# Kernel tuning notes

Hardware: AMD Instinct MI355X
Metric: run time of the kernel (lower is better)

## Reference

```python
import jax, jax.numpy as jnp
import numpy as np

VOXEL_SIZE = 0.4
GAMMA = 1.1  # VoxelPointsSampler.GAMMA
PC_MIN, PC_MAX = -75.2, 75.2


def setup_inputs() -> dict:
    key = jax.random.key(0)
    ks = jax.random.split(key, 6)
    N, M, C, S = 200000, 256, 5, 128
    xy = jax.random.uniform(ks[0], (N, 2), minval=PC_MIN, maxval=PC_MAX)
    z = jax.random.uniform(ks[1], (N, 1), minval=-2.0, maxval=4.0)
    feat = jax.random.normal(ks[2], (N, C - 3))
    points = jnp.concatenate([xy, z, feat], axis=1)  # [N, 5]
    ctr = jax.random.uniform(ks[3], (M, 2), minval=PC_MIN * 0.9, maxval=PC_MAX * 0.9)
    cz = jnp.zeros((M, 1), jnp.float32)
    dims = jax.random.uniform(ks[4], (M, 3), minval=1.0, maxval=5.0)
    yaw = jax.random.uniform(ks[5], (M, 1), minval=-3.14, maxval=3.14)
    boxes = jnp.concatenate([ctr, cz, dims, yaw], axis=1)  # [M, 7]
    pc_start = jnp.array([PC_MIN, PC_MIN], dtype=jnp.float32)
    return {"points": points, "boxes": boxes, "pc_start": pc_start, "num_sample": S}


def reference(points, boxes, pc_start, num_sample):
    N, C = points.shape
    M = boxes.shape[0]
    # --- voxel-level radius ball query (distances in voxel units) ---
    pcoords = (points[:, :2] - pc_start) / VOXEL_SIZE          # [N, 2]
    qcoords = (boxes[:, :2] - pc_start) / VOXEL_SIZE           # [M, 2]
    r_vox = jnp.linalg.norm(boxes[:, 3:5] * 0.5, axis=-1) * GAMMA / VOXEL_SIZE  # [M]
    dist = jnp.linalg.norm(qcoords[:, None, :] - pcoords[None, :, :], axis=-1)  # [M, N]
    vmask = (dist < r_vox[:, None]).any(axis=0)                # [N]
    # --- cylindrical pool (metric space); invalid points pushed out of every radius ---
    BIG = jnp.asarray(1e6, points.dtype)
    xy_m = jnp.where(vmask[:, None], points[:, :2], BIG)       # [N, 2]
    radii = jnp.linalg.norm(boxes[:, 3:5] * 0.5, axis=-1) * GAMMA  # [M]
    dis = jnp.linalg.norm(boxes[:, None, :2] - xy_m[None, :, :], axis=-1)  # [M, N]
    pmask = (dis <= radii[:, None]).astype(points.dtype)       # 0/1 [M, N]
    sm, sidx = jax.lax.top_k(pmask, num_sample)                # [M, S]
    smb = sm > 0.5                                             # bool [M, S]
    # unique indices across all sampled slots (fixed-size for jit)
    uniq, inv = jnp.unique(sidx.ravel(), return_inverse=True,
                           size=M * num_sample, fill_value=0)
    query_points = points[uniq]                                # [M*S, C] (padded)
    sampled_points = points[sidx] * smb[:, :, None]            # [M, S, C]
    idx = inv.reshape(M, num_sample).astype(jnp.int32) * smb   # [M, S]
    return sampled_points, idx, query_points
```

## Files before the change

kernel.cpp:

```cpp
#include <hip/hip_runtime.h>

typedef unsigned long long u64;
typedef unsigned short u16;
typedef unsigned char u8;

#define VOX 0.4f
#define GAM 1.1f
#define NCX 16
#define CELLW 32.0f
#define CAP 64

__device__ __forceinline__ float dist2d(float ax, float ay, float bx, float by) {
  float dx = __fsub_rn(ax, bx);
  float dy = __fsub_rn(ay, by);
  return __fsqrt_rn(__fadd_rn(__fmul_rn(dx, dx), __fmul_rn(dy, dy)));
}

__device__ __forceinline__ float box_radius(const float* __restrict__ boxes, int m) {
  float hx = __fmul_rn(boxes[m * 7 + 3], 0.5f);
  float hy = __fmul_rn(boxes[m * 7 + 4], 0.5f);
  float nr = __fsqrt_rn(__fadd_rn(__fmul_rn(hx, hx), __fmul_rn(hy, hy)));
  return __fmul_rn(nr, GAM);
}

__device__ __forceinline__ void box_voxel(const float* __restrict__ boxes, int m,
                                          float psx, float psy,
                                          float& qx, float& qy, float& r) {
  qx = __fdiv_rn(__fsub_rn(boxes[m * 7 + 0], psx), VOX);
  qy = __fdiv_rn(__fsub_rn(boxes[m * 7 + 1], psy), VOX);
  float hx = __fmul_rn(boxes[m * 7 + 3], 0.5f);
  float hy = __fmul_rn(boxes[m * 7 + 4], 0.5f);
  float nr = __fsqrt_rn(__fadd_rn(__fmul_rn(hx, hx), __fmul_rn(hy, hy)));
  r = __fdiv_rn(__fmul_rn(nr, GAM), VOX);
}

__global__ void k_prep(const float* __restrict__ boxes, const float* __restrict__ pc_start,
                       float* __restrict__ qxv, float* __restrict__ qyv, float* __restrict__ rv,
                       int* __restrict__ cellCnt, u16* __restrict__ cellList, int M) {
  const int tid = threadIdx.x;
  if (blockIdx.x == 0) {
    for (int m = tid; m < M; m += 256) {
      float qx, qy, r;
      box_voxel(boxes, m, pc_start[0], pc_start[1], qx, qy, r);
      qxv[m] = qx; qyv[m] = qy; rv[m] = r;
    }
    return;
  }
  const int cell = blockIdx.x - 1;
  const int cx = cell & (NCX - 1), cy = cell >> 4;
  const int wv = tid >> 6, lane = tid & 63;
  __shared__ int wcnt[4];
  const float x0 = (cx == 0) ? -3e38f : cx * CELLW;
  const float x1 = (cx == NCX - 1) ? 3e38f : (cx + 1) * CELLW;
  const float y0 = (cy == 0) ? -3e38f : cy * CELLW;
  const float y1 = (cy == NCX - 1) ? 3e38f : (cy + 1) * CELLW;
  bool hit = false;
  if (tid < M) {
    float qx, qy, r;
    box_voxel(boxes, tid, pc_start[0], pc_start[1], qx, qy, r);
    float ddx = fmaxf(0.0f, fmaxf(x0 - qx, qx - x1));
    float ddy = fmaxf(0.0f, fmaxf(y0 - qy, qy - y1));
    float rr = r + 0.01f;
    hit = (ddx * ddx + ddy * ddy <= rr * rr);
  }
  u64 b = __ballot(hit);
  if (lane == 0) wcnt[wv] = __popcll(b);
  __syncthreads();
  int base = 0;
  for (int w = 0; w < wv; ++w) base += wcnt[w];
  if (hit) {
    int slot = base + __popcll(b & ((1ULL << lane) - 1ULL));
    if (slot < CAP) cellList[cell * CAP + slot] = (u16)tid;
  }
  if (tid == 0) cellCnt[cell] = wcnt[0] + wcnt[1] + wcnt[2] + wcnt[3];
}

__global__ void k_vmask_count(const float* __restrict__ pts, const float* __restrict__ boxes,
                              const float* __restrict__ qxv, const float* __restrict__ qyv,
                              const float* __restrict__ rv,
                              const int* __restrict__ cellCnt, const u16* __restrict__ cellList,
                              u64* __restrict__ vbits, u8* __restrict__ present,
                              u64* __restrict__ bmG, int* __restrict__ cpng,
                              const float* __restrict__ pc_start,
                              int N, int M) {
  __shared__ float cpx[256], cpy[256];
  __shared__ int cpn[256];
  __shared__ float sbx[256], sby[256], sbr[256];
  __shared__ u64 bm[256][4];
  __shared__ int wcnt[4];
  const int tid = threadIdx.x;
  const int blk = blockIdx.x;
  const int n = blk * 256 + tid;
  const int wv = tid >> 6, lane = tid & 63;
  const float psx = pc_start[0], psy = pc_start[1];
  const bool valid = (n < N);

  bm[tid][0] = 0; bm[tid][1] = 0; bm[tid][2] = 0; bm[tid][3] = 0;
  if (tid < M) {
    sbx[tid] = boxes[tid * 7 + 0];
    sby[tid] = boxes[tid * 7 + 1];
    sbr[tid] = box_radius(boxes, tid);
  }

  float px = 1e6f, py = 1e6f, pvx = 0.f, pvy = 0.f;
  if (valid) {
    px = pts[n * 5 + 0];
    py = pts[n * 5 + 1];
    pvx = __fdiv_rn(__fsub_rn(px, psx), VOX);
    pvy = __fdiv_rn(__fsub_rn(py, psy), VOX);
    present[n] = 0;
  }

  bool flag = false;
  if (valid) {
    int cx = (int)floorf(pvx * (1.0f / CELLW));
    int cy = (int)floorf(pvy * (1.0f / CELLW));
    cx = cx < 0 ? 0 : (cx > NCX - 1 ? NCX - 1 : cx);
    cy = cy < 0 ? 0 : (cy > NCX - 1 ? NCX - 1 : cy);
    const int cell = cy * NCX + cx;
    const int k = cellCnt[cell];
    if (k <= CAP) {
      for (int j = 0; j < k; ++j) {
        const int m = cellList[cell * CAP + j];
        float d = dist2d(qxv[m], qyv[m], pvx, pvy);
        if (d < rv[m]) { flag = true; break; }
      }
    } else {
      for (int m = 0; m < M; ++m) {
        float d = dist2d(qxv[m], qyv[m], pvx, pvy);
        if (d < rv[m]) { flag = true; break; }
      }
    }
  }
  u64 b = __ballot(flag);
  if (lane == 0) {
    vbits[n >> 6] = b;
    wcnt[wv] = __popcll(b);
  }
  __syncthreads();

  int base = 0;
  for (int w = 0; w < wv; ++w) base += wcnt[w];
  if (flag) {
    int slot = base + __popcll(b & ((1ULL << lane) - 1ULL));
    cpx[slot] = px;
    cpy[slot] = py;
    cpn[slot] = n;
  }
  __syncthreads();
  const int nfl = wcnt[0] + wcnt[1] + wcnt[2] + wcnt[3];
  if (tid < nfl) cpng[blk * 256 + tid] = cpn[tid];

  if (tid < nfl) {
    const float mx = cpx[tid], my = cpy[tid];
    float vx = __fdiv_rn(__fsub_rn(mx, psx), VOX);
    float vy = __fdiv_rn(__fsub_rn(my, psy), VOX);
    int cx = (int)floorf(vx * (1.0f / CELLW));
    int cy = (int)floorf(vy * (1.0f / CELLW));
    cx = cx < 0 ? 0 : (cx > NCX - 1 ? NCX - 1 : cx);
    cy = cy < 0 ? 0 : (cy > NCX - 1 ? NCX - 1 : cy);
    const int cell = cy * NCX + cx;
    const int k = cellCnt[cell];
    const u64 bit = 1ULL << (tid & 63);
    const int word = tid >> 6;
    if (k <= CAP) {
      for (int j = 0; j < k; ++j) {
        const int m = cellList[cell * CAP + j];
        float d = dist2d(sbx[m], sby[m], mx, my);
        if (d <= sbr[m]) atomicOr(&bm[m][word], bit);
      }
    } else {
      for (int m = 0; m < M; ++m) {
        float d = dist2d(sbx[m], sby[m], mx, my);
        if (d <= sbr[m]) atomicOr(&bm[m][word], bit);
      }
    }
  }
  __syncthreads();

  if (tid < M) {
    u64* dst = bmG + ((size_t)blk * M + tid) * 4;
    dst[0] = bm[tid][0]; dst[1] = bm[tid][1];
    dst[2] = bm[tid][2]; dst[3] = bm[tid][3];
  }
}

__global__ void __launch_bounds__(1024) k_scanfill(
    const float* __restrict__ pts, const float* __restrict__ boxes,
    const u64* __restrict__ bmG, const int* __restrict__ cpng,
    const u64* __restrict__ vbits, int* __restrict__ kcount,
    int* __restrict__ sidx, u8* __restrict__ present,
    int N, int M, int S, int nchunk) {
  const int m = blockIdx.x;
  const int t = threadIdx.x;
  const int lane = t & 63, wv = t >> 6;
  __shared__ int wsum[16];
  __shared__ int zws[16];

  u64 w0 = 0, w1 = 0, w2 = 0, w3 = 0;
  int v = 0;
  if (t < nchunk) {
    const u64* bp = bmG + ((size_t)t * M + m) * 4;
    w0 = bp[0]; w1 = bp[1]; w2 = bp[2]; w3 = bp[3];
    v = __popcll(w0) + __popcll(w1) + __popcll(w2) + __popcll(w3);
  }
  int incl = v;
  for (int d = 1; d < 64; d <<= 1) {
    int x = __shfl_up(incl, d);
    if (lane >= d) incl += x;
  }
  if (lane == 63) wsum[wv] = incl;
  __syncthreads();
  if (t < 16) {
    int s = wsum[t];
    for (int d = 1; d < 16; d <<= 1) {
      int x = __shfl_up(s, d);
      if (t >= d) s += x;
    }
    wsum[t] = s;
  }
  __syncthreads();
  const int wbase = (wv > 0) ? wsum[wv - 1] : 0;
  const int off = wbase + incl - v;
  const int total = wsum[15];
  const int k0 = total < S ? total : S;
  if (t == 0) kcount[m] = k0;

  if (t < nchunk && v > 0 && off < S) {
    const int* pbase = cpng + t * 256;
    int cum = off;
    u64 ws4[4] = {w0, w1, w2, w3};
    for (int wi = 0; wi < 4 && cum < S; ++wi) {
      u64 w = ws4[wi];
      while (w && cum < S) {
        int j = (wi << 6) + __builtin_ctzll(w);
        w &= w - 1;
        int pn = pbase[j];
        sidx[m * S + cum] = pn;
        present[pn] = 1;
        ++cum;
      }
    }
  }

  if (k0 >= S) return;
  const float bx = boxes[m * 7 + 0], by = boxes[m * 7 + 1];
  const float r = box_radius(boxes, m);
  const u64 ltmask = (1ULL << lane) - 1ULL;
  int fill = k0;
  for (int p0 = 0; p0 < N && fill < S; p0 += 1024) {
    const int n = p0 + t;
    const bool validn = n < N;
    bool one = false;
    if (validn) {
      u64 wbit = vbits[n >> 6];
      if ((wbit >> (n & 63)) & 1ULL) {
        float d = dist2d(bx, by, pts[n * 5 + 0], pts[n * 5 + 1]);
        one = (d <= r);
      }
    }
    const bool z = validn && !one;
    u64 b = __ballot(z);
    if (lane == 0) zws[wv] = __popcll(b);
    __syncthreads();
    int zbase = 0, ztot = 0;
    for (int ww = 0; ww < 16; ++ww) {
      int c = zws[ww];
      if (ww < wv) zbase += c;
      ztot += c;
    }
    if (z) {
      int pos = fill + zbase + __popcll(b & ltmask);
      if (pos < S) { sidx[m * S + pos] = n; present[n] = 1; }
    }
    fill += ztot;
    __syncthreads();
  }
}

__global__ void k_bsum(const u8* __restrict__ present, int* __restrict__ bsum, int N) {
  const int n = blockIdx.x * 256 + threadIdx.x;
  bool f = (n < N) && present[n];
  u64 b = __ballot(f);
  __shared__ int ws[4];
  if ((threadIdx.x & 63) == 0) ws[threadIdx.x >> 6] = __popcll(b);
  __syncthreads();
  if (threadIdx.x == 0) bsum[blockIdx.x] = ws[0] + ws[1] + ws[2] + ws[3];
}

__global__ void __launch_bounds__(1024) k_scan(const int* __restrict__ bsum,
                                               int* __restrict__ boff, int nb) {
  __shared__ int s[1024];
  const int t = threadIdx.x;
  int v = (t < nb) ? bsum[t] : 0;
  s[t] = v;
  __syncthreads();
  for (int d = 1; d < 1024; d <<= 1) {
    int x = (t >= d) ? s[t - d] : 0;
    __syncthreads();
    s[t] += x;
    __syncthreads();
  }
  boff[t] = s[t] - v;
  if (t == nb - 1) boff[1024] = s[t];
}

__global__ void k_rank(const u8* __restrict__ present, const int* __restrict__ boff,
                       const float* __restrict__ pts, int* __restrict__ rank_arr,
                       float* __restrict__ out_query, int N) {
  const int t = threadIdx.x;
  const int n = blockIdx.x * 256 + t;
  bool f = (n < N) && present[n];
  u64 b = __ballot(f);
  __shared__ int ws[4];
  const int wv = t >> 6, lane = t & 63;
  if (lane == 0) ws[wv] = __popcll(b);
  __syncthreads();
  int base = boff[blockIdx.x];
  for (int w = 0; w < wv; ++w) base += ws[w];
  if (f) {
    int rank = base + __popcll(b & ((1ULL << lane) - 1ULL));
    rank_arr[n] = rank;
    float* q = out_query + (size_t)rank * 5;
    const float* p = pts + (size_t)n * 5;
    q[0] = p[0]; q[1] = p[1]; q[2] = p[2]; q[3] = p[3]; q[4] = p[4];
  }
}

__global__ void k_outpad(const float* __restrict__ pts, const int* __restrict__ sidx,
                         const int* __restrict__ kcount, const int* __restrict__ rank_arr,
                         const int* __restrict__ uptr,
                         float* __restrict__ out_samp, float* __restrict__ out_idx,
                         float* __restrict__ out_query, int MS, int S) {
  const int e = blockIdx.x * 256 + threadIdx.x;
  if (e >= MS) return;
  const int U = *uptr;
  if (e >= U) {
    float* q = out_query + (size_t)e * 5;
    q[0] = pts[0]; q[1] = pts[1]; q[2] = pts[2]; q[3] = pts[3]; q[4] = pts[4];
  }
  const int m = e / S;
  const int s = e - m * S;
  float* o = out_samp + (size_t)e * 5;
  if (s < kcount[m]) {
    int n = sidx[e];
    const float* p = pts + (size_t)n * 5;
    o[0] = p[0]; o[1] = p[1]; o[2] = p[2]; o[3] = p[3]; o[4] = p[4];
    out_idx[e] = (float)rank_arr[n];
  } else {
    o[0] = 0.f; o[1] = 0.f; o[2] = 0.f; o[3] = 0.f; o[4] = 0.f;
    out_idx[e] = 0.f;
  }
}

extern "C" void kernel_launch(void* const* d_in, const int* in_sizes, int n_in,
                              void* d_out, int out_size, void* d_ws, size_t ws_size,
                              hipStream_t stream) {
  const float* pts = (const float*)d_in[0];
  const float* boxes = (const float*)d_in[1];
  const float* pc_start = (const float*)d_in[2];
  const int N = in_sizes[0] / 5;
  const int M = in_sizes[1] / 7;
  const int S = out_size / (M * 11);
  const int MS = M * S;

  float* out_samp = (float*)d_out;
  float* out_idx = out_samp + (size_t)MS * 5;
  float* out_query = out_idx + (size_t)MS;

  const int nb = (N + 255) / 256;
  const int nchunk = nb;

  char* w = (char*)d_ws;
  auto take = [&](size_t bytes) {
    char* p = w;
    w += (bytes + 15) & ~(size_t)15;
    return (void*)p;
  };
  u64* vbits     = (u64*)take((size_t)(nb * 4) * 8);
  u64* bmG       = (u64*)take((size_t)nchunk * M * 4 * 8);
  int* cpng      = (int*)take((size_t)nchunk * 256 * 4);
  int* sidx      = (int*)take((size_t)MS * 4);
  int* kcount    = (int*)take((size_t)M * 4);
  int* rank_arr  = (int*)take((size_t)N * 4);
  int* bsum      = (int*)take((size_t)1024 * 4);
  int* boff      = (int*)take((size_t)1025 * 4);
  u8*  present   = (u8*)take((size_t)N);
  float* qxv     = (float*)take((size_t)M * 4);
  float* qyv     = (float*)take((size_t)M * 4);
  float* rv      = (float*)take((size_t)M * 4);
  int* cellCnt   = (int*)take((size_t)NCX * NCX * 4);
  u16* cellList  = (u16*)take((size_t)NCX * NCX * CAP * 2);

  k_prep<<<NCX * NCX + 1, 256, 0, stream>>>(boxes, pc_start, qxv, qyv, rv,
                                            cellCnt, cellList, M);
  k_vmask_count<<<nb, 256, 0, stream>>>(pts, boxes, qxv, qyv, rv, cellCnt, cellList,
                                        vbits, present, bmG, cpng, pc_start, N, M);
  k_scanfill<<<M, 1024, 0, stream>>>(pts, boxes, bmG, cpng, vbits, kcount,
                                     sidx, present, N, M, S, nchunk);
  k_bsum<<<nb, 256, 0, stream>>>(present, bsum, N);
  k_scan<<<1, 1024, 0, stream>>>(bsum, boff, nb);
  k_rank<<<nb, 256, 0, stream>>>(present, boff, pts, rank_arr, out_query, N);
  k_outpad<<<(MS + 255) / 256, 256, 0, stream>>>(pts, sidx, kcount, rank_arr, boff + 1024,
                                                 out_samp, out_idx, out_query, MS, S);
}
```

Measured before the change: 94.77 us.

## Merge block-sum and scan into one kernel, transpose bitmask layout, cache cell ids

Replaces the separate per-block present-count kernel and single-block scan with one 1024-thread kernel. It popcounts the present bytes four at a time and scans them with wave shuffles, which removes one launch and one global round trip. The per-box bitmask array is transposed to box-major order, so each scanfill block reads its chunks contiguously instead of with a stride of M. The voxel cell of each flagged point is kept in shared memory rather than recomputed. The cost is that one block now reads all 200K present bytes serially, with less parallelism than before.

```diff
diff --git a/kernel.cpp b/kernel.cpp
--- a/kernel.cpp
+++ b/kernel.cpp
@@ -1,6 +1,7 @@
 #include <hip/hip_runtime.h>
 
 typedef unsigned long long u64;
+typedef unsigned int u32;
 typedef unsigned short u16;
 typedef unsigned char u8;
 
@@ -82,9 +83,10 @@
                               u64* __restrict__ vbits, u8* __restrict__ present,
                               u64* __restrict__ bmG, int* __restrict__ cpng,
                               const float* __restrict__ pc_start,
-                              int N, int M) {
+                              int N, int M, int nchunk) {
   __shared__ float cpx[256], cpy[256];
   __shared__ int cpn[256];
+  __shared__ int ccell[256];
   __shared__ float sbx[256], sby[256], sbr[256];
   __shared__ u64 bm[256][4];
   __shared__ int wcnt[4];
@@ -112,16 +114,17 @@
   }
 
   bool flag = false;
+  int mycell = 0;
   if (valid) {
     int cx = (int)floorf(pvx * (1.0f / CELLW));
     int cy = (int)floorf(pvy * (1.0f / CELLW));
     cx = cx < 0 ? 0 : (cx > NCX - 1 ? NCX - 1 : cx);
     cy = cy < 0 ? 0 : (cy > NCX - 1 ? NCX - 1 : cy);
-    const int cell = cy * NCX + cx;
-    const int k = cellCnt[cell];
+    mycell = cy * NCX + cx;
+    const int k = cellCnt[mycell];
     if (k <= CAP) {
       for (int j = 0; j < k; ++j) {
-        const int m = cellList[cell * CAP + j];
+        const int m = cellList[mycell * CAP + j];
         float d = dist2d(qxv[m], qyv[m], pvx, pvy);
         if (d < rv[m]) { flag = true; break; }
       }
@@ -146,6 +149,7 @@
     cpx[slot] = px;
     cpy[slot] = py;
     cpn[slot] = n;
+    ccell[slot] = mycell;
   }
   __syncthreads();
   const int nfl = wcnt[0] + wcnt[1] + wcnt[2] + wcnt[3];
@@ -153,13 +157,7 @@
 
   if (tid < nfl) {
     const float mx = cpx[tid], my = cpy[tid];
-    float vx = __fdiv_rn(__fsub_rn(mx, psx), VOX);
-    float vy = __fdiv_rn(__fsub_rn(my, psy), VOX);
-    int cx = (int)floorf(vx * (1.0f / CELLW));
-    int cy = (int)floorf(vy * (1.0f / CELLW));
-    cx = cx < 0 ? 0 : (cx > NCX - 1 ? NCX - 1 : cx);
-    cy = cy < 0 ? 0 : (cy > NCX - 1 ? NCX - 1 : cy);
-    const int cell = cy * NCX + cx;
+    const int cell = ccell[tid];
     const int k = cellCnt[cell];
     const u64 bit = 1ULL << (tid & 63);
     const int word = tid >> 6;
@@ -179,7 +177,7 @@
   __syncthreads();
 
   if (tid < M) {
-    u64* dst = bmG + ((size_t)blk * M + tid) * 4;
+    u64* dst = bmG + ((size_t)tid * nchunk + blk) * 4;
     dst[0] = bm[tid][0]; dst[1] = bm[tid][1];
     dst[2] = bm[tid][2]; dst[3] = bm[tid][3];
   }
@@ -200,7 +198,7 @@
   u64 w0 = 0, w1 = 0, w2 = 0, w3 = 0;
   int v = 0;
   if (t < nchunk) {
-    const u64* bp = bmG + ((size_t)t * M + m) * 4;
+    const u64* bp = bmG + ((size_t)m * nchunk + t) * 4;
     w0 = bp[0]; w1 = bp[1]; w2 = bp[2]; w3 = bp[3];
     v = __popcll(w0) + __popcll(w1) + __popcll(w2) + __popcll(w3);
   }
@@ -278,31 +276,45 @@
   }
 }
 
-__global__ void k_bsum(const u8* __restrict__ present, int* __restrict__ bsum, int N) {
-  const int n = blockIdx.x * 256 + threadIdx.x;
-  bool f = (n < N) && present[n];
-  u64 b = __ballot(f);
-  __shared__ int ws[4];
-  if ((threadIdx.x & 63) == 0) ws[threadIdx.x >> 6] = __popcll(b);
-  __syncthreads();
-  if (threadIdx.x == 0) bsum[blockIdx.x] = ws[0] + ws[1] + ws[2] + ws[3];
-}
-
-__global__ void __launch_bounds__(1024) k_scan(const int* __restrict__ bsum,
-                                               int* __restrict__ boff, int nb) {
-  __shared__ int s[1024];
-  const int t = threadIdx.x;
-  int v = (t < nb) ? bsum[t] : 0;
-  s[t] = v;
-  __syncthreads();
-  for (int d = 1; d < 1024; d <<= 1) {
-    int x = (t >= d) ? s[t - d] : 0;
-    __syncthreads();
-    s[t] += x;
-    __syncthreads();
-  }
-  boff[t] = s[t] - v;
-  if (t == nb - 1) boff[1024] = s[t];
+__global__ void __launch_bounds__(1024) k_sumscan(const u8* __restrict__ present,
+                                                  int* __restrict__ boff, int N, int nb) {
+  __shared__ int cs[1024];
+  __shared__ int wsum[16];
+  const int t = threadIdx.x, lane = t & 63, wv = t >> 6;
+  const u32* p32 = (const u32*)present;
+  for (int c = wv; c < nb; c += 16) {
+    const int idx = c * 64 + lane;
+    const int byte0 = idx * 4;
+    int s = 0;
+    if (byte0 + 3 < N) {
+      s = __popc(p32[idx] & 0x01010101u);
+    } else {
+      for (int bb = byte0; bb < N; ++bb) s += present[bb];
+    }
+    for (int d = 32; d > 0; d >>= 1) s += __shfl_down(s, d);
+    if (lane == 0) cs[c] = s;
+  }
+  __syncthreads();
+  int v = (t < nb) ? cs[t] : 0;
+  int incl = v;
+  for (int d = 1; d < 64; d <<= 1) {
+    int x = __shfl_up(incl, d);
+    if (lane >= d) incl += x;
+  }
+  if (lane == 63) wsum[wv] = incl;
+  __syncthreads();
+  if (t < 16) {
+    int s = wsum[t];
+    for (int d = 1; d < 16; d <<= 1) {
+      int x = __shfl_up(s, d);
+      if (t >= d) s += x;
+    }
+    wsum[t] = s;
+  }
+  __syncthreads();
+  const int base = (wv > 0) ? wsum[wv - 1] : 0;
+  if (t < nb) boff[t] = base + incl - v;
+  if (t == 0) boff[1024] = wsum[15];
 }
 
 __global__ void k_rank(const u8* __restrict__ present, const int* __restrict__ boff,
@@ -378,12 +390,11 @@
     return (void*)p;
   };
   u64* vbits     = (u64*)take((size_t)(nb * 4) * 8);
-  u64* bmG       = (u64*)take((size_t)nchunk * M * 4 * 8);
+  u64* bmG       = (u64*)take((size_t)M * nchunk * 4 * 8);
   int* cpng      = (int*)take((size_t)nchunk * 256 * 4);
   int* sidx      = (int*)take((size_t)MS * 4);
   int* kcount    = (int*)take((size_t)M * 4);
   int* rank_arr  = (int*)take((size_t)N * 4);
-  int* bsum      = (int*)take((size_t)1024 * 4);
   int* boff      = (int*)take((size_t)1025 * 4);
   u8*  present   = (u8*)take((size_t)N);
   float* qxv     = (float*)take((size_t)M * 4);
@@ -395,11 +406,10 @@
   k_prep<<<NCX * NCX + 1, 256, 0, stream>>>(boxes, pc_start, qxv, qyv, rv,
                                             cellCnt, cellList, M);
   k_vmask_count<<<nb, 256, 0, stream>>>(pts, boxes, qxv, qyv, rv, cellCnt, cellList,
-                                        vbits, present, bmG, cpng, pc_start, N, M);
+                                        vbits, present, bmG, cpng, pc_start, N, M, nchunk);
   k_scanfill<<<M, 1024, 0, stream>>>(pts, boxes, bmG, cpng, vbits, kcount,
                                      sidx, present, N, M, S, nchunk);
-  k_bsum<<<nb, 256, 0, stream>>>(present, bsum, N);
-  k_scan<<<1, 1024, 0, stream>>>(bsum, boff, nb);
+  k_sumscan<<<1, 1024, 0, stream>>>(present, boff, N, nb);
   k_rank<<<nb, 256, 0, stream>>>(present, boff, pts, rank_arr, out_query, N);
   k_outpad<<<(MS + 255) / 256, 256, 0, stream>>>(pts, sidx, kcount, rank_arr, boff + 1024,
                                                  out_samp, out_idx, out_query, MS, S);
```

New measurement: 114.2 us. +20.5%, slower.
